# Optimization experiments

Measured on AMD Instinct MI355X. Metric: run time of the kernel, lower is better.

Reference implementation:

```python
import jax, jax.numpy as jnp
import numpy as np

NUM_HEADS = 4
NUM_POINTS = 8


def setup_inputs() -> dict:
    key0 = jax.random.key(0)
    ks = jax.random.split(key0, 14)
    B, S, N, D, C = 1, 6, 10000, 4, 128
    Hf, Wf = 46, 80
    M = Hf * Wf
    HP2 = NUM_HEADS * NUM_POINTS * 2
    HP = NUM_HEADS * NUM_POINTS
    inp = {
        "query": jax.random.normal(ks[0], (B, N, C), jnp.float32),
        "key": jax.random.normal(ks[1], (S, M, B, C), jnp.float32),
        "value": jax.random.normal(ks[2], (S, M, B, C), jnp.float32),
        "query_pos": jax.random.normal(ks[3], (B, N, C), jnp.float32),
        "reference_points_cam": jax.random.uniform(ks[4], (S, B, N, D, 2), jnp.float32),
        "Wv": jax.random.normal(ks[5], (C, C), jnp.float32) * 0.02,
        "bv": jnp.zeros((C,), jnp.float32),
        "Wo": jax.random.normal(ks[6], (C, HP2), jnp.float32) * 0.02,
        "bo": jax.random.normal(ks[7], (HP2,), jnp.float32) * 0.5,
        "Wa": jax.random.normal(ks[8], (C, HP), jnp.float32) * 0.02,
        "ba": jnp.zeros((HP,), jnp.float32),
        "Wp": jax.random.normal(ks[9], (C, C), jnp.float32) * 0.02,
        "bp": jnp.zeros((C,), jnp.float32),
        "spatial_shapes": np.array([[Hf, Wf]], dtype=np.int64),
        "bev_mask": jax.random.uniform(ks[10], (S, B, N, D)) < 0.3,
    }
    return inp


def _bilinear_sample(value_hw, loc, Hf, Wf):
    # value_hw: [BS, H, Hf*Wf, Dh]; loc: [BS, L, H, P, 2] normalized to [0,1]
    # grid_sample(align_corners=False, padding=zeros) semantics: ix = x*W - 0.5
    x = loc[..., 0] * Wf - 0.5
    y = loc[..., 1] * Hf - 0.5
    x0 = jnp.floor(x)
    y0 = jnp.floor(y)
    lx = x - x0
    ly = y - y0
    x0i = x0.astype(jnp.int32)
    y0i = y0.astype(jnp.int32)

    BS, L, H, P = x.shape
    Dh = value_hw.shape[-1]

    def gat(xi, yi):
        valid = (xi >= 0) & (xi < Wf) & (yi >= 0) & (yi < Hf)
        idx = jnp.clip(yi, 0, Hf - 1) * Wf + jnp.clip(xi, 0, Wf - 1)  # [BS,L,H,P]
        idx_t = idx.transpose(0, 2, 1, 3).reshape(BS, H, L * P)
        v = jnp.take_along_axis(value_hw, idx_t[..., None], axis=2)  # [BS,H,L*P,Dh]
        v = v.reshape(BS, H, L, P, Dh)
        return v * valid.transpose(0, 2, 1, 3)[..., None]

    def wt(w):  # [BS,L,H,P] -> [BS,H,L,P,1]
        return w.transpose(0, 2, 1, 3)[..., None]

    out = (gat(x0i, y0i) * wt((1 - lx) * (1 - ly))
           + gat(x0i + 1, y0i) * wt(lx * (1 - ly))
           + gat(x0i, y0i + 1) * wt((1 - lx) * ly)
           + gat(x0i + 1, y0i + 1) * wt(lx * ly))
    return out  # [BS,H,L,P,Dh]


def _deform_attn(q, val, ref, Hf, Wf, Wv, bv, Wo, bo, Wa, ba):
    # q: [BS,L,C], val: [BS,M,C], ref: [BS,L,D,2]
    BS, L, C = q.shape
    Dh = C // NUM_HEADS
    D = ref.shape[2]
    value_p = (val @ Wv + bv).reshape(BS, -1, NUM_HEADS, Dh)
    value_hw = value_p.transpose(0, 2, 1, 3)  # [BS,H,M,Dh]

    off = (q @ Wo + bo).reshape(BS, L, NUM_HEADS, NUM_POINTS, 2)
    attw = jax.nn.softmax((q @ Wa + ba).reshape(BS, L, NUM_HEADS, NUM_POINTS), axis=-1)

    normalizer = jnp.array([Wf, Hf], dtype=q.dtype)  # (x_norm, y_norm)
    off = off / normalizer
    # split points into (points_per_Z, num_Z_anchors) and add per-anchor reference
    off = off.reshape(BS, L, NUM_HEADS, NUM_POINTS // D, D, 2)
    loc = ref[:, :, None, None, :, :] + off  # [BS,L,H,P//D,D,2]
    loc = loc.reshape(BS, L, NUM_HEADS, NUM_POINTS, 2)

    sampled = _bilinear_sample(value_hw, loc, Hf, Wf)  # [BS,H,L,P,Dh]
    out = jnp.einsum('bhlpd,blhp->blhd', sampled, attw)
    return out.reshape(BS, L, C)


def reference(query, key, value, query_pos, reference_points_cam,
              Wv, bv, Wo, bo, Wa, ba, Wp, bp, spatial_shapes, bev_mask):
    B, N, C = query.shape
    S, M = key.shape[0], key.shape[1]
    Hf = int(spatial_shapes[0][0])
    Wf = int(spatial_shapes[0][1])

    q = query + query_pos
    # dense equivalent of the per-camera nonzero() rebatch: run deformable
    # attention for every (batch, camera, query), then mask + scatter-add.
    q_bs = jnp.broadcast_to(q[:, None], (B, S, N, C)).reshape(B * S, N, C)
    ref_bs = reference_points_cam.transpose(1, 0, 2, 3, 4).reshape(B * S, N, -1, 2)
    val_bs = value.transpose(2, 0, 1, 3).reshape(B * S, M, C)

    out = _deform_attn(q_bs, val_bs, ref_bs, Hf, Wf, Wv, bv, Wo, bo, Wa, ba)
    out = out.reshape(B, S, N, C)

    mask_q = (bev_mask.sum(-1) > 0)            # [S,B,N] query visible in camera
    mask_q = mask_q.transpose(1, 0, 2)         # [B,S,N]
    slots = jnp.einsum('bsnc,bsn->bnc', out, mask_q.astype(out.dtype))
    count = jnp.maximum(mask_q.sum(1).astype(out.dtype), 1.0)  # [B,N]
    slots = slots / count[..., None]
    # dropout in eval mode is identity
    return slots @ Wp + bp + query
```

## Files before the change

### kernel.cpp

```cpp
#include <hip/hip_runtime.h>


#define S_DIM 6
#define N_DIM 10000
#define C_DIM 128
#define M_DIM 3680
#define H_DIM 4
#define P_DIM 8
#define DH    32
#define HF    46
#define WF    80

#define G_Q   4
#define NENT  (S_DIM * H_DIM * P_DIM)
#define VHW_SHORTS (S_DIM * H_DIM * M_DIM * DH)

__device__ __forceinline__ float bf2f(unsigned short u) {
    return __uint_as_float(((unsigned)u) << 16);
}
__device__ __forceinline__ unsigned short f2bf(float f) {
    unsigned b = __float_as_uint(f);
    b += 0x7FFFu + ((b >> 16) & 1u);
    return (unsigned short)(b >> 16);
}

__global__ __launch_bounds__(128) void vproj_kernel(
    const float* __restrict__ value,
    const float* __restrict__ Wv,
    const float* __restrict__ bv,
    unsigned short* __restrict__ vhw)
{
    const int row0 = blockIdx.x * 16;
    const int t = threadIdx.x;
    __shared__ float vs[16][C_DIM];

#pragma unroll
    for (int i = 0; i < 16; ++i)
        vs[i][t] = value[(size_t)(row0 + i) * C_DIM + t];
    __syncthreads();

    float acc[16];
#pragma unroll
    for (int i = 0; i < 16; ++i) acc[i] = 0.f;

    for (int k = 0; k < C_DIM; k += 4) {
        const float w0 = Wv[(k + 0) * C_DIM + t];
        const float w1 = Wv[(k + 1) * C_DIM + t];
        const float w2 = Wv[(k + 2) * C_DIM + t];
        const float w3 = Wv[(k + 3) * C_DIM + t];
#pragma unroll
        for (int i = 0; i < 16; ++i) {
            const float4 v = *(const float4*)&vs[i][k];
            acc[i] = fmaf(v.x, w0, acc[i]);
            acc[i] = fmaf(v.y, w1, acc[i]);
            acc[i] = fmaf(v.z, w2, acc[i]);
            acc[i] = fmaf(v.w, w3, acc[i]);
        }
    }
    const float b = bv[t];
    const int h = t >> 5, dh = t & 31;
#pragma unroll
    for (int i = 0; i < 16; ++i) {
        const int row = row0 + i;
        const int s = row / M_DIM;
        const int m = row - s * M_DIM;
        vhw[(((size_t)s * H_DIM + h) * M_DIM + m) * DH + dh] = f2bf(acc[i] + b);
    }
}

__global__ __launch_bounds__(256, 4) void attn_kernel(
    const unsigned short* __restrict__ vhw,
    const float* __restrict__ query,
    const float* __restrict__ query_pos,
    const float* __restrict__ Wo, const float* __restrict__ bo,
    const float* __restrict__ Wa, const float* __restrict__ ba,
    const float* __restrict__ refpts,
    const void* __restrict__ bev_mask,
    const void* __restrict__ sshapes,
    const float* __restrict__ Wp, const float* __restrict__ bp,
    float* __restrict__ out)
{
    const int n0 = blockIdx.x * G_Q;
    const int t = threadIdx.x;

    __shared__ float qs[G_Q][C_DIM];
    __shared__ float s_offr[G_Q][64];
    __shared__ float s_ar[G_Q][32];
    __shared__ float s_attw[G_Q][32];
    __shared__ float s_w[G_Q][NENT][4];
    __shared__ int   s_o[G_Q][NENT][4];
    __shared__ float s_slots[G_Q][C_DIM];
    __shared__ int   s_mask[G_Q][S_DIM];
    __shared__ float s_inv[G_Q];

    for (int i = t; i < G_Q * C_DIM; i += 256) {
        const int g = i >> 7, c = i & 127;
        const size_t a = (size_t)(n0 + g) * C_DIM + c;
        qs[g][c] = query[a] + query_pos[a];
    }
    if (t < G_Q * S_DIM) {
        const int g = t / S_DIM, s = t - g * S_DIM;
        const int n = n0 + g;
        const int* ss32 = (const int*)sshapes;
        const bool i32mode = (ss32[1] == WF);
        int mk;
        if (i32mode) {
            const int* bm = (const int*)bev_mask + ((size_t)s * N_DIM + n) * 4;
            mk = (bm[0] | bm[1] | bm[2] | bm[3]) ? 1 : 0;
        } else {
            const unsigned char* bm =
                (const unsigned char*)bev_mask + ((size_t)s * N_DIM + n) * 4;
            mk = (bm[0] | bm[1] | bm[2] | bm[3]) ? 1 : 0;
        }
        s_mask[g][s] = mk;
    }
    __syncthreads();
    if (t < G_Q) {
        int c = 0;
#pragma unroll
        for (int s = 0; s < S_DIM; ++s) c += s_mask[t][s];
        s_inv[t] = 1.f / fmaxf((float)c, 1.f);
    }

    {
        const int g = t >> 6, j = t & 63;
        float acc = 0.f;
        for (int k = 0; k < C_DIM; k += 4) {
            const float4 q4 = *(const float4*)&qs[g][k];
            acc = fmaf(q4.x, Wo[(k + 0) * 64 + j], acc);
            acc = fmaf(q4.y, Wo[(k + 1) * 64 + j], acc);
            acc = fmaf(q4.z, Wo[(k + 2) * 64 + j], acc);
            acc = fmaf(q4.w, Wo[(k + 3) * 64 + j], acc);
        }
        s_offr[g][j] = acc + bo[j];
    }
    if (t < G_Q * 32) {
        const int g = t >> 5, jj = t & 31;
        float acc = 0.f;
        for (int k = 0; k < C_DIM; k += 4) {
            const float4 q4 = *(const float4*)&qs[g][k];
            acc = fmaf(q4.x, Wa[(k + 0) * 32 + jj], acc);
            acc = fmaf(q4.y, Wa[(k + 1) * 32 + jj], acc);
            acc = fmaf(q4.z, Wa[(k + 2) * 32 + jj], acc);
            acc = fmaf(q4.w, Wa[(k + 3) * 32 + jj], acc);
        }
        s_ar[g][jj] = acc + ba[jj];
    }
    __syncthreads();
    if (t < G_Q * 32) {
        const int g = t >> 5, hp = t & 31;
        const float v = s_ar[g][hp];
        float m = v;
        for (int d = 1; d < 8; d <<= 1) m = fmaxf(m, __shfl_xor(m, d, 8));
        const float e = expf(v - m);
        float sum = e;
        for (int d = 1; d < 8; d <<= 1) sum += __shfl_xor(sum, d, 8);
        s_attw[g][hp] = e / sum;
    }
    __syncthreads();

    for (int i = t; i < G_Q * NENT; i += 256) {
        const int g = i / NENT, e = i - g * NENT;
        const int s = e >> 5, hp = e & 31;
        const int p = hp & 7, eh = hp >> 3, d = p & 3;
        const int n = n0 + g;

        const float aw = s_attw[g][hp];
        const float offx = s_offr[g][hp * 2 + 0] / (float)WF;
        const float offy = s_offr[g][hp * 2 + 1] / (float)HF;
        const float refx = refpts[(((size_t)s * N_DIM + n) * 4 + d) * 2 + 0];
        const float refy = refpts[(((size_t)s * N_DIM + n) * 4 + d) * 2 + 1];

        const float x = (refx + offx) * (float)WF - 0.5f;
        const float y = (refy + offy) * (float)HF - 0.5f;
        const float x0f = floorf(x), y0f = floorf(y);
        const float lx = x - x0f, ly = y - y0f;
        const int x0 = (int)x0f, y0 = (int)y0f;
        const int x1 = x0 + 1, y1 = y0 + 1;

        const bool vx0 = (x0 >= 0) & (x0 < WF);
        const bool vx1 = (x1 >= 0) & (x1 < WF);
        const bool vy0 = (y0 >= 0) & (y0 < HF);
        const bool vy1 = (y1 >= 0) & (y1 < HF);

        const int cx0 = min(max(x0, 0), WF - 1);
        const int cx1 = min(max(x1, 0), WF - 1);
        const int cy0 = min(max(y0, 0), HF - 1);
        const int cy1 = min(max(y1, 0), HF - 1);

        const int base = (s * H_DIM + eh) * M_DIM;
        const int r0 = base + cy0 * WF;
        const int r1 = base + cy1 * WF;
        s_o[g][e][0] = (r0 + cx0) * (DH * 2);
        s_o[g][e][1] = (r0 + cx1) * (DH * 2);
        s_o[g][e][2] = (r1 + cx0) * (DH * 2);
        s_o[g][e][3] = (r1 + cx1) * (DH * 2);

        const float wx0 = 1.f - lx, wy0 = 1.f - ly;
        s_w[g][e][0] = (vx0 & vy0) ? wx0 * wy0 * aw : 0.f;
        s_w[g][e][1] = (vx1 & vy0) ? lx  * wy0 * aw : 0.f;
        s_w[g][e][2] = (vx0 & vy1) ? wx0 * ly  * aw : 0.f;
        s_w[g][e][3] = (vx1 & vy1) ? lx  * ly  * aw : 0.f;
    }
    __syncthreads();

    {
        const char* vb = (const char*)vhw;
        const int local = t & 127, qsel = t >> 7;
        const int h = local >> 5, dh2 = (local & 31) * 2;
#pragma unroll
        for (int gp = 0; gp < 2; ++gp) {
            const int g = gp * 2 + qsel;
            float acc = 0.f;
            for (int s = 0; s < S_DIM; ++s) {
                if (!s_mask[g][s]) continue;
                const int eb = s * 32 + h * 8;
#pragma unroll
                for (int pg = 0; pg < 2; ++pg) {
                    unsigned short r[16];
#pragma unroll
                    for (int p = 0; p < 4; ++p) {
                        const int4 o = *(const int4*)s_o[g][eb + pg * 4 + p];
                        r[p * 4 + 0] = *(const unsigned short*)(vb + (o.x + dh2));
                        r[p * 4 + 1] = *(const unsigned short*)(vb + (o.y + dh2));
                        r[p * 4 + 2] = *(const unsigned short*)(vb + (o.z + dh2));
                        r[p * 4 + 3] = *(const unsigned short*)(vb + (o.w + dh2));
                    }
#pragma unroll
                    for (int p = 0; p < 4; ++p) {
                        const float4 w = *(const float4*)s_w[g][eb + pg * 4 + p];
                        acc = fmaf(w.x, bf2f(r[p * 4 + 0]), acc);
                        acc = fmaf(w.y, bf2f(r[p * 4 + 1]), acc);
                        acc = fmaf(w.z, bf2f(r[p * 4 + 2]), acc);
                        acc = fmaf(w.w, bf2f(r[p * 4 + 3]), acc);
                    }
                }
            }
            s_slots[g][local] = acc * s_inv[g];
        }
    }
    __syncthreads();

    {
        const int c = t & 127, half = t >> 7;
        const int g0 = half * 2;
        float a0 = 0.f, a1 = 0.f;
        for (int k = 0; k < C_DIM; k += 4) {
            const float4 s0 = *(const float4*)&s_slots[g0][k];
            const float4 s1 = *(const float4*)&s_slots[g0 + 1][k];
            const float w0 = Wp[(k + 0) * C_DIM + c];
            const float w1 = Wp[(k + 1) * C_DIM + c];
            const float w2 = Wp[(k + 2) * C_DIM + c];
            const float w3 = Wp[(k + 3) * C_DIM + c];
            a0 = fmaf(s0.x, w0, a0); a1 = fmaf(s1.x, w0, a1);
            a0 = fmaf(s0.y, w1, a0); a1 = fmaf(s1.y, w1, a1);
            a0 = fmaf(s0.z, w2, a0); a1 = fmaf(s1.z, w2, a1);
            a0 = fmaf(s0.w, w3, a0); a1 = fmaf(s1.w, w3, a1);
        }
        const int na = n0 + g0;
        const float bb = bp[c];
        out[(size_t)na * C_DIM + c]       = a0 + bb + query[(size_t)na * C_DIM + c];
        out[(size_t)(na + 1) * C_DIM + c] = a1 + bb + query[(size_t)(na + 1) * C_DIM + c];
    }
}

extern "C" void kernel_launch(void* const* d_in, const int* in_sizes, int n_in,
                              void* d_out, int out_size, void* d_ws, size_t ws_size,
                              hipStream_t stream) {
    const float* query     = (const float*)d_in[0];
    const float* value     = (const float*)d_in[2];
    const float* query_pos = (const float*)d_in[3];
    const float* refpts    = (const float*)d_in[4];
    const float* Wv        = (const float*)d_in[5];
    const float* bv        = (const float*)d_in[6];
    const float* Wo        = (const float*)d_in[7];
    const float* bo        = (const float*)d_in[8];
    const float* Wa        = (const float*)d_in[9];
    const float* ba        = (const float*)d_in[10];
    const float* Wp        = (const float*)d_in[11];
    const float* bp        = (const float*)d_in[12];
    const void*  sshapes   = d_in[13];
    const void*  bev_mask  = d_in[14];

    unsigned short* vhw = (unsigned short*)d_ws;
    float* outp = (float*)d_out;

    hipLaunchKernelGGL(vproj_kernel, dim3((S_DIM * M_DIM) / 16), dim3(128), 0, stream,
                       value, Wv, bv, vhw);
    hipLaunchKernelGGL(attn_kernel, dim3(N_DIM / G_Q), dim3(256), 0, stream,
                       vhw, query, query_pos, Wo, bo, Wa, ba,
                       refpts, bev_mask, sshapes, Wp, bp, outp);
}
```

Measured before the change: 89.50 us.

## Gather two bf16 channels per load and map one wave per query

The bilinear gather now reads a 32-bit word (two bf16 channels) per tap instead of a single 16-bit value. Each 64-lane wave handles one query, with 16 lanes per head covering 32 channels. The shared offset and weight tables are reordered to [s][p][h] as int4/float4, so lanes of different heads read adjacent entries. This halves the number of gather instructions and avoids the duplicated weight and offset reads of the old two-pass loop. Each thread now carries two accumulators and issues eight loads per step.

Result: faster. 84.49 us (-5.6%).

```diff
diff --git a/kernel.cpp b/kernel.cpp
--- a/kernel.cpp
+++ b/kernel.cpp
@@ -12,11 +12,14 @@
 #define WF    80
 
 #define G_Q   4
-#define NENT  (S_DIM * H_DIM * P_DIM)
+#define NENT  (S_DIM * P_DIM * H_DIM)
 #define VHW_SHORTS (S_DIM * H_DIM * M_DIM * DH)
 
-__device__ __forceinline__ float bf2f(unsigned short u) {
-    return __uint_as_float(((unsigned)u) << 16);
+__device__ __forceinline__ float bfl(unsigned u) {
+    return __uint_as_float(u << 16);
+}
+__device__ __forceinline__ float bfh(unsigned u) {
+    return __uint_as_float(u & 0xffff0000u);
 }
 __device__ __forceinline__ unsigned short f2bf(float f) {
     unsigned b = __float_as_uint(f);
@@ -83,15 +86,15 @@
     const int n0 = blockIdx.x * G_Q;
     const int t = threadIdx.x;
 
-    __shared__ float qs[G_Q][C_DIM];
-    __shared__ float s_offr[G_Q][64];
-    __shared__ float s_ar[G_Q][32];
-    __shared__ float s_attw[G_Q][32];
-    __shared__ float s_w[G_Q][NENT][4];
-    __shared__ int   s_o[G_Q][NENT][4];
-    __shared__ float s_slots[G_Q][C_DIM];
-    __shared__ int   s_mask[G_Q][S_DIM];
-    __shared__ float s_inv[G_Q];
+    __shared__ float  qs[G_Q][C_DIM];
+    __shared__ float  s_offr[G_Q][64];
+    __shared__ float  s_ar[G_Q][32];
+    __shared__ float  s_attw[G_Q][32];
+    __shared__ int4   s_o[G_Q][S_DIM][P_DIM][H_DIM];
+    __shared__ float4 s_w[G_Q][S_DIM][P_DIM][H_DIM];
+    __shared__ float  s_slots[G_Q][C_DIM];
+    __shared__ int    s_mask[G_Q][S_DIM];
+    __shared__ float  s_inv[G_Q];
 
     for (int i = t; i < G_Q * C_DIM; i += 256) {
         const int g = i >> 7, c = i & 127;
@@ -160,9 +163,13 @@
     __syncthreads();
 
     for (int i = t; i < G_Q * NENT; i += 256) {
-        const int g = i / NENT, e = i - g * NENT;
-        const int s = e >> 5, hp = e & 31;
-        const int p = hp & 7, eh = hp >> 3, d = p & 3;
+        const int g = i / NENT;
+        const int e = i - g * NENT;
+        const int s = e >> 5;
+        const int rem = e & 31;
+        const int p = rem >> 2, h = rem & 3;
+        const int hp = h * P_DIM + p;
+        const int d = p & 3;
         const int n = n0 + g;
 
         const float aw = s_attw[g][hp];
@@ -188,56 +195,59 @@
         const int cy0 = min(max(y0, 0), HF - 1);
         const int cy1 = min(max(y1, 0), HF - 1);
 
-        const int base = (s * H_DIM + eh) * M_DIM;
+        const int base = (s * H_DIM + h) * M_DIM;
         const int r0 = base + cy0 * WF;
         const int r1 = base + cy1 * WF;
-        s_o[g][e][0] = (r0 + cx0) * (DH * 2);
-        s_o[g][e][1] = (r0 + cx1) * (DH * 2);
-        s_o[g][e][2] = (r1 + cx0) * (DH * 2);
-        s_o[g][e][3] = (r1 + cx1) * (DH * 2);
+        s_o[g][s][p][h] = make_int4((r0 + cx0) * (DH * 2),
+                                    (r0 + cx1) * (DH * 2),
+                                    (r1 + cx0) * (DH * 2),
+                                    (r1 + cx1) * (DH * 2));
 
         const float wx0 = 1.f - lx, wy0 = 1.f - ly;
-        s_w[g][e][0] = (vx0 & vy0) ? wx0 * wy0 * aw : 0.f;
-        s_w[g][e][1] = (vx1 & vy0) ? lx  * wy0 * aw : 0.f;
-        s_w[g][e][2] = (vx0 & vy1) ? wx0 * ly  * aw : 0.f;
-        s_w[g][e][3] = (vx1 & vy1) ? lx  * ly  * aw : 0.f;
+        s_w[g][s][p][h] = make_float4((vx0 & vy0) ? wx0 * wy0 * aw : 0.f,
+                                      (vx1 & vy0) ? lx  * wy0 * aw : 0.f,
+                                      (vx0 & vy1) ? wx0 * ly  * aw : 0.f,
+                                      (vx1 & vy1) ? lx  * ly  * aw : 0.f);
     }
     __syncthreads();
 
     {
         const char* vb = (const char*)vhw;
-        const int local = t & 127, qsel = t >> 7;
-        const int h = local >> 5, dh2 = (local & 31) * 2;
-#pragma unroll
-        for (int gp = 0; gp < 2; ++gp) {
-            const int g = gp * 2 + qsel;
-            float acc = 0.f;
-            for (int s = 0; s < S_DIM; ++s) {
-                if (!s_mask[g][s]) continue;
-                const int eb = s * 32 + h * 8;
-#pragma unroll
-                for (int pg = 0; pg < 2; ++pg) {
-                    unsigned short r[16];
-#pragma unroll
-                    for (int p = 0; p < 4; ++p) {
-                        const int4 o = *(const int4*)s_o[g][eb + pg * 4 + p];
-                        r[p * 4 + 0] = *(const unsigned short*)(vb + (o.x + dh2));
-                        r[p * 4 + 1] = *(const unsigned short*)(vb + (o.y + dh2));
-                        r[p * 4 + 2] = *(const unsigned short*)(vb + (o.z + dh2));
-                        r[p * 4 + 3] = *(const unsigned short*)(vb + (o.w + dh2));
-                    }
-#pragma unroll
-                    for (int p = 0; p < 4; ++p) {
-                        const float4 w = *(const float4*)s_w[g][eb + pg * 4 + p];
-                        acc = fmaf(w.x, bf2f(r[p * 4 + 0]), acc);
-                        acc = fmaf(w.y, bf2f(r[p * 4 + 1]), acc);
-                        acc = fmaf(w.z, bf2f(r[p * 4 + 2]), acc);
-                        acc = fmaf(w.w, bf2f(r[p * 4 + 3]), acc);
-                    }
-                }
+        const int g = t >> 6;
+        const int lane = t & 63;
+        const int h = lane >> 4;
+        const int dhp4 = (lane & 15) * 4;
+        float accx = 0.f, accy = 0.f;
+
+        for (int s = 0; s < S_DIM; ++s) {
+            if (!s_mask[g][s]) continue;
+#pragma unroll
+            for (int pg = 0; pg < 4; ++pg) {
+                const int4 o0 = s_o[g][s][pg * 2 + 0][h];
+                const int4 o1 = s_o[g][s][pg * 2 + 1][h];
+                unsigned u0 = *(const unsigned*)(vb + (o0.x + dhp4));
+                unsigned u1 = *(const unsigned*)(vb + (o0.y + dhp4));
+                unsigned u2 = *(const unsigned*)(vb + (o0.z + dhp4));
+                unsigned u3 = *(const unsigned*)(vb + (o0.w + dhp4));
+                unsigned u4 = *(const unsigned*)(vb + (o1.x + dhp4));
+                unsigned u5 = *(const unsigned*)(vb + (o1.y + dhp4));
+                unsigned u6 = *(const unsigned*)(vb + (o1.z + dhp4));
+                unsigned u7 = *(const unsigned*)(vb + (o1.w + dhp4));
+                const float4 w0 = s_w[g][s][pg * 2 + 0][h];
+                const float4 w1 = s_w[g][s][pg * 2 + 1][h];
+                accx = fmaf(w0.x, bfl(u0), accx); accy = fmaf(w0.x, bfh(u0), accy);
+                accx = fmaf(w0.y, bfl(u1), accx); accy = fmaf(w0.y, bfh(u1), accy);
+                accx = fmaf(w0.z, bfl(u2), accx); accy = fmaf(w0.z, bfh(u2), accy);
+                accx = fmaf(w0.w, bfl(u3), accx); accy = fmaf(w0.w, bfh(u3), accy);
+                accx = fmaf(w1.x, bfl(u4), accx); accy = fmaf(w1.x, bfh(u4), accy);
+                accx = fmaf(w1.y, bfl(u5), accx); accy = fmaf(w1.y, bfh(u5), accy);
+                accx = fmaf(w1.z, bfl(u6), accx); accy = fmaf(w1.z, bfh(u6), accy);
+                accx = fmaf(w1.w, bfl(u7), accx); accy = fmaf(w1.w, bfh(u7), accy);
             }
-            s_slots[g][local] = acc * s_inv[g];
-        }
+        }
+        const float inv = s_inv[g];
+        *(float2*)&s_slots[g][h * 32 + (lane & 15) * 2] =
+            make_float2(accx * inv, accy * inv);
     }
     __syncthreads();
 
```
